# Kernel tuning notes

Measured on AMD Instinct MI355X. Metric: run time of the kernel, lower is better.

Reference implementation:

```python
import jax, jax.numpy as jnp
import numpy as np

N_NODES = 100000
N_EDGES = 1600000
N_GRAPHS = 256
HIDDEN = 256
ADD_FEATURES = 7
BN_EPS = 1e-5


def setup_inputs() -> dict:
    key = jax.random.key(0)
    ks = jax.random.split(key, 12)
    x = jax.random.normal(ks[0], (N_NODES, 1), dtype=jnp.float32)
    edge_index = jax.random.randint(ks[1], (2, N_EDGES), 0, N_NODES, dtype=jnp.int32)
    batch = jnp.sort(jax.random.randint(ks[2], (N_NODES,), 0, N_GRAPHS, dtype=jnp.int32))
    y_feat = jax.random.normal(ks[3], (N_GRAPHS, ADD_FEATURES), dtype=jnp.float32)
    # learned parameters
    W_conv = jax.random.normal(ks[4], (1, HIDDEN), dtype=jnp.float32) * 0.5
    b_conv = jnp.zeros((HIDDEN,), dtype=jnp.float32)
    gamma = jnp.ones((HIDDEN,), dtype=jnp.float32)
    beta = jnp.zeros((HIDDEN,), dtype=jnp.float32)
    W1 = jax.random.normal(ks[5], (HIDDEN + ADD_FEATURES, 128), dtype=jnp.float32) * (1.0 / np.sqrt(HIDDEN + ADD_FEATURES))
    b1 = jnp.zeros((128,), dtype=jnp.float32)
    W2 = jax.random.normal(ks[6], (128, 2), dtype=jnp.float32) * (1.0 / np.sqrt(128))
    b2 = jnp.zeros((2,), dtype=jnp.float32)
    return {"x": x, "edge_index": edge_index, "batch": batch, "y_feat": y_feat,
            "W_conv": W_conv, "b_conv": b_conv, "gamma": gamma, "beta": beta,
            "W1": W1, "b1": b1, "W2": W2, "b2": b2}


def _gcn_conv(x, W, b, edge_index, n_nodes):
    # PyG GCNConv: add self-loops, symmetric normalization D^-1/2 (A+I) D^-1/2 (x W) + b
    loop = jnp.arange(n_nodes, dtype=edge_index.dtype)
    src = jnp.concatenate([edge_index[0], loop])
    dst = jnp.concatenate([edge_index[1], loop])
    deg = jax.ops.segment_sum(jnp.ones_like(dst, dtype=x.dtype), dst, num_segments=n_nodes)
    dinv = jnp.where(deg > 0, jax.lax.rsqrt(jnp.maximum(deg, 1e-12)), 0.0)
    norm = dinv[src] * dinv[dst]                      # [E+N]
    xw = x @ W                                        # [N, H]
    msg = xw[src] * norm[:, None]                     # gather [E+N, H]
    return jax.ops.segment_sum(msg, dst, num_segments=n_nodes) + b


def reference(x, edge_index, batch, y_feat, W_conv, b_conv, gamma, beta, W1, b1, W2, b2):
    n_nodes = x.shape[0]
    h = _gcn_conv(x, W_conv, b_conv, edge_index, n_nodes)      # [N, 256]
    h = jax.nn.gelu(h, approximate=False)
    # BatchNorm over nodes (training-mode batch stats, biased variance, eps=1e-5)
    mean = jnp.mean(h, axis=0)
    var = jnp.mean(jnp.square(h - mean), axis=0)
    h = (h - mean) * jax.lax.rsqrt(var + BN_EPS) * gamma + beta
    # global mean pool by graph id
    sums = jax.ops.segment_sum(h, batch, num_segments=N_GRAPHS)           # [G, 256]
    counts = jax.ops.segment_sum(jnp.ones((n_nodes,), h.dtype), batch, num_segments=N_GRAPHS)
    pooled = sums / jnp.maximum(counts, 1.0)[:, None]
    g = jnp.concatenate([pooled, y_feat], axis=1)               # [G, 263]
    g = jax.nn.gelu(g @ W1 + b1, approximate=False)             # [G, 128]
    out = jax.nn.sigmoid(g @ W2 + b2)                           # [G, 2]
    return out
```

## Files before the change

### kernel.cpp

```cpp
#include <hip/hip_runtime.h>
#include <hip/hip_bf16.h>

#define HID 256
#define ADDF 7
#define MLP1 128
#define BN_EPS 1e-5f
#define NREP 8

#define NB 512
#define BW 196
#define BCAP 4096
#define NW 4
#define NR 8
#define NCHUNK 512

__device__ __forceinline__ float gelu_fast(float z) {
    float z2 = z * z;
    float y2 = z * fmaf(0.07135481627f, z2, 1.59576912161f);
    float u  = __expf(fminf(y2, 80.0f));
    return z * u * __builtin_amdgcn_rcpf(u + 1.0f);
}

__global__ __launch_bounds__(256) void k_hist(
        const int* __restrict__ dst, int* __restrict__ hist,
        float* __restrict__ zbase, int zcount, int E, int nchunk, int cpx, int PC) {
    __shared__ int h[NW][NB];
    const int t = threadIdx.x;
    const int bid = blockIdx.x;

    for (int gt = bid * 256 + t; gt < zcount; gt += (int)gridDim.x * 256) zbase[gt] = 0.0f;

    const int m = (bid & 7) * cpx + (bid >> 3);
    for (int k = t; k < NW * NB; k += 256) (&h[0][0])[k] = 0;
    __syncthreads();

    if (m < nchunk) {
        const int s0 = m * PC;
        const int e0 = min(s0 + PC, E);
        const int w = t >> 6;
        const bool al = ((((uintptr_t)(dst + s0)) & 15) == 0);
        const int n4 = al ? ((e0 - s0) >> 2) : 0;
        const int4* dst4 = (const int4*)(dst + s0);
        for (int q = t; q < n4; q += 256) {
            int4 d = dst4[q];
            atomicAdd(&h[w][d.x / BW], 1);
            atomicAdd(&h[w][d.y / BW], 1);
            atomicAdd(&h[w][d.z / BW], 1);
            atomicAdd(&h[w][d.w / BW], 1);
        }
        for (int i = s0 + (n4 << 2) + t; i < e0; i += 256)
            atomicAdd(&h[w][dst[i] / BW], 1);
        __syncthreads();
        for (int b = t; b < NB; b += 256)
            hist[(size_t)m * NB + b] = h[0][b] + h[1][b] + h[2][b] + h[3][b];
    }
}

__global__ __launch_bounds__(64) void k_scan(
        int* __restrict__ hist, int* __restrict__ binCur,
        const int* __restrict__ batch, int* __restrict__ cnt,
        int nchunk, int N, int G) {
    const int bin = blockIdx.x;
    const int lane = threadIdx.x;
    __shared__ int bounds[2];

    if (bin < G && lane < 2) {
        int target = bin + lane;
        int lo = 0, hi = N;
        while (lo < hi) { int mid = (lo + hi) >> 1; if (batch[mid] < target) lo = mid + 1; else hi = mid; }
        bounds[lane] = lo;
    }

    const int per = (nchunk + 63) / 64;
    const int m0 = lane * per;
    const int m1 = min(m0 + per, nchunk);
    int sum = 0;
    for (int m = m0; m < m1; ++m) sum += hist[(size_t)m * NB + bin];

    int incl = sum;
    #pragma unroll
    for (int d = 1; d < 64; d <<= 1) {
        int o = __shfl_up(incl, d);
        if (lane >= d) incl += o;
    }
    const int total = __shfl(incl, 63);
    int run = bin * BCAP + (incl - sum);
    for (int m = m0; m < m1; ++m) {
        int c = hist[(size_t)m * NB + bin];
        hist[(size_t)m * NB + bin] = run;
        run += c;
    }
    if (lane == 63) binCur[bin] = bin * BCAP + total;

    __syncthreads();
    if (bin < G && lane == 0) cnt[bin] = bounds[1] - bounds[0];
}

__global__ __launch_bounds__(256) void k_store(
        const int* __restrict__ src, const int* __restrict__ dst,
        const int* __restrict__ hist, int* __restrict__ recs,
        int E, int nchunk, int cpx, int PC) {
    __shared__ int cur[NB];
    const int t = threadIdx.x;
    const int m = ((int)blockIdx.x & 7) * cpx + ((int)blockIdx.x >> 3);
    if (m >= nchunk) return;

    {
        const int4* hrow = (const int4*)(hist + (size_t)m * NB);
        int4* cur4 = (int4*)cur;
        for (int b = t; b < NB / 4; b += 256) cur4[b] = hrow[b];
    }
    __syncthreads();

    const int s0 = m * PC;
    const int e0 = min(s0 + PC, E);
    const bool al = (((((uintptr_t)(dst + s0)) | ((uintptr_t)(src + s0))) & 15) == 0);
    const int n4 = al ? ((e0 - s0) >> 2) : 0;
    const int4* dst4 = (const int4*)(dst + s0);
    const int4* src4 = (const int4*)(src + s0);
    for (int q = t; q < n4; q += 256) {
        int4 d = dst4[q];
        int4 s = src4[q];
        int bin, pos;
        bin = d.x / BW; pos = atomicAdd(&cur[bin], 1); recs[pos] = ((d.x - bin * BW) << 17) | s.x;
        bin = d.y / BW; pos = atomicAdd(&cur[bin], 1); recs[pos] = ((d.y - bin * BW) << 17) | s.y;
        bin = d.z / BW; pos = atomicAdd(&cur[bin], 1); recs[pos] = ((d.z - bin * BW) << 17) | s.z;
        bin = d.w / BW; pos = atomicAdd(&cur[bin], 1); recs[pos] = ((d.w - bin * BW) << 17) | s.w;
    }
    for (int i = s0 + (n4 << 2) + t; i < e0; i += 256) {
        int d = dst[i];
        int bin = d / BW;
        int pos = atomicAdd(&cur[bin], 1);
        recs[pos] = ((d - bin * BW) << 17) | src[i];
    }
}

__global__ __launch_bounds__(1024) void k_degv(
        const int* __restrict__ recs, const int* __restrict__ binCur,
        const float* __restrict__ x, float* __restrict__ dinv, float* __restrict__ v, int N) {
    __shared__ int degL[NR][BW];
    const int b = blockIdx.x;
    const int t = threadIdx.x;
    const int rp = t >> 7;
    for (int k = t; k < NR * BW; k += 1024) (&degL[0][0])[k] = 0;
    __syncthreads();

    const int start = b * BCAP;
    const int end   = binCur[b];
    const int n4 = (end - start) >> 2;
    const int4* r4 = (const int4*)(recs + start);
    for (int q = t; q < n4; q += 1024) {
        int4 r = r4[q];
        atomicAdd(&degL[rp][r.x >> 17], 1);
        atomicAdd(&degL[rp][r.y >> 17], 1);
        atomicAdd(&degL[rp][r.z >> 17], 1);
        atomicAdd(&degL[rp][r.w >> 17], 1);
    }
    for (int i = start + (n4 << 2) + t; i < end; i += 1024)
        atomicAdd(&degL[rp][recs[i] >> 17], 1);
    __syncthreads();

    int node = b * BW + t;
    if (t < BW && node < N) {
        int d = 0;
        #pragma unroll
        for (int r = 0; r < NR; ++r) d += degL[r][t];
        float di = rsqrtf((float)d + 1.0f);
        dinv[node] = di;
        v[node]    = di * x[node];
    }
}

__global__ __launch_bounds__(1024) void k_agg_gelu(
        const int* __restrict__ recs, const int* __restrict__ binCur,
        const float* __restrict__ v, const float* __restrict__ dinv,
        const int* __restrict__ batch,
        const float* __restrict__ Wc, const float* __restrict__ bc,
        float* __restrict__ Sgj, float* __restrict__ Trep, float* __restrict__ T2rep, int N) {
    __shared__ float aggL[NR][BW];
    __shared__ float sh_s[BW];
    __shared__ int   sh_b[BW];
    const int b = blockIdx.x;
    const int t = threadIdx.x;
    const int rp = t >> 7;
    for (int k = t; k < NR * BW; k += 1024) (&aggL[0][0])[k] = 0.0f;
    __syncthreads();

    const int start = b * BCAP;
    const int end   = binCur[b];
    const int n4 = (end - start) >> 2;
    const int4* r4 = (const int4*)(recs + start);
    for (int q = t; q < n4; q += 1024) {
        int4 r = r4[q];
        atomicAdd(&aggL[rp][r.x >> 17], v[r.x & 0x1FFFF]);
        atomicAdd(&aggL[rp][r.y >> 17], v[r.y & 0x1FFFF]);
        atomicAdd(&aggL[rp][r.z >> 17], v[r.z & 0x1FFFF]);
        atomicAdd(&aggL[rp][r.w >> 17], v[r.w & 0x1FFFF]);
    }
    for (int i = start + (n4 << 2) + t; i < end; i += 1024) {
        int rec = recs[i];
        atomicAdd(&aggL[rp][rec >> 17], v[rec & 0x1FFFF]);
    }
    __syncthreads();

    const int node0 = b * BW;
    const int count = min(BW, N - node0);
    if (count <= 0) return;

    if (t < count) {
        int node = node0 + t;
        float a = 0.f;
        #pragma unroll
        for (int r = 0; r < NR; ++r) a += aggL[r][t];
        sh_s[t] = dinv[node] * (a + v[node]);
        sh_b[t] = batch[node];
    }
    __syncthreads();

    const int f = t & 255;
    const int qg = t >> 8;
    const int nbeg = qg * 49;
    const int nend = min(nbeg + 49, count);
    if (nbeg < nend) {
        const float wa = Wc[f];
        const float wb = bc[f];
        float tsum = 0.f, t2sum = 0.f, gsum = 0.f;
        int gid = sh_b[nbeg];
        int n = nbeg;
        for (; n + 2 <= nend; n += 2) {
            float h0 = gelu_fast(fmaf(sh_s[n],     wa, wb));
            float h1 = gelu_fast(fmaf(sh_s[n + 1], wa, wb));
            int b0 = sh_b[n], b1v = sh_b[n + 1];
            tsum += h0 + h1; t2sum += fmaf(h0, h0, h1 * h1);
            if (b0 != gid)  { atomicAdd(&Sgj[gid * HID + f], gsum); gsum = 0.f; gid = b0; }
            gsum += h0;
            if (b1v != gid) { atomicAdd(&Sgj[gid * HID + f], gsum); gsum = 0.f; gid = b1v; }
            gsum += h1;
        }
        if (n < nend) {
            float h0 = gelu_fast(fmaf(sh_s[n], wa, wb));
            tsum += h0; t2sum += h0 * h0;
            int b0 = sh_b[n];
            if (b0 != gid) { atomicAdd(&Sgj[gid * HID + f], gsum); gsum = 0.f; gid = b0; }
            gsum += h0;
        }
        atomicAdd(&Sgj[gid * HID + f], gsum);
        const int r = (b * 4 + qg) & (NREP - 1);
        atomicAdd(&Trep [r * HID + f], tsum);
        atomicAdd(&T2rep[r * HID + f], t2sum);
    }
}

__global__ __launch_bounds__(HID) void k_pool_mlp(
        const float* __restrict__ Sgj, const float* __restrict__ Trep, const float* __restrict__ T2rep,
        const int* __restrict__ cnt, const float* __restrict__ gamma, const float* __restrict__ beta,
        const float* __restrict__ yfeat,
        const float* __restrict__ W1, const float* __restrict__ b1,
        const float* __restrict__ W2, const float* __restrict__ b2,
        float* __restrict__ out, int N) {
    __shared__ float gv[HID + ADDF];
    __shared__ float hid[MLP1];
    const int g = blockIdx.x;
    const int t = threadIdx.x;

    float Ts = 0.f, T2s = 0.f;
    #pragma unroll
    for (int r = 0; r < NREP; ++r) { Ts += Trep[r * HID + t]; T2s += T2rep[r * HID + t]; }
    float invN = 1.0f / (float)N;
    float mean = Ts * invN;
    float var  = fmaf(-mean, mean, T2s * invN);
    float rinv = rsqrtf(var + BN_EPS);
    float c = (float)max(cnt[g], 1);
    gv[t] = (Sgj[g * HID + t] / c - mean) * rinv * gamma[t] + beta[t];
    if (t < ADDF) gv[HID + t] = yfeat[g * ADDF + t];
    __syncthreads();

    if (t < MLP1) {
        float acc = b1[t];
        #pragma unroll 8
        for (int k = 0; k < HID + ADDF; ++k)
            acc = fmaf(gv[k], W1[k * MLP1 + t], acc);
        hid[t] = gelu_fast(acc);
    }
    __syncthreads();

    if (t < 2) {
        float o = b2[t];
        for (int k = 0; k < MLP1; ++k)
            o = fmaf(hid[k], W2[k * 2 + t], o);
        out[g * 2 + t] = 1.0f / (1.0f + expf(-o));
    }
}

__global__ void k_init_fb(float* zp, int nz, const int* __restrict__ batch,
                          int* __restrict__ cnt, int N, int G) {
    const int nzBlocks = (nz + 255) / 256;
    if ((int)blockIdx.x < nzBlocks) {
        int i = blockIdx.x * 256 + threadIdx.x;
        if (i < nz) zp[i] = 0.0f;
    } else {
        const int t = threadIdx.x;
        if (t < G) {
            int lo = 0, hi = N;
            while (lo < hi) { int mid = (lo + hi) >> 1; if (batch[mid] < t) lo = mid + 1; else hi = mid; }
            int start = lo;
            lo = 0; hi = N;
            while (lo < hi) { int mid = (lo + hi) >> 1; if (batch[mid] < t + 1) lo = mid + 1; else hi = mid; }
            cnt[t] = lo - start;
        }
    }
}
__global__ void k_zero(float* p, int n) {
    for (int i = blockIdx.x * blockDim.x + threadIdx.x; i < n; i += gridDim.x * blockDim.x)
        p[i] = 0.0f;
}
__global__ void k_deg_fb(const int* __restrict__ dst, float* __restrict__ deg, int E) {
    int i = blockIdx.x * blockDim.x + threadIdx.x;
    if (i < E) atomicAdd(&deg[dst[i]], 1.0f);
}
__global__ void k_dinv_fb(float* __restrict__ deg, const float* __restrict__ x,
                          float* __restrict__ v, int N) {
    int i = blockIdx.x * blockDim.x + threadIdx.x;
    if (i < N) { float di = rsqrtf(deg[i] + 1.0f); deg[i] = di; v[i] = di * x[i]; }
}
__global__ void k_scatter_fb(const int* __restrict__ src, const int* __restrict__ dst,
                             const float* __restrict__ v, float* __restrict__ agg, int E) {
    int i = blockIdx.x * blockDim.x + threadIdx.x;
    if (i < E) atomicAdd(&agg[dst[i]], v[src[i]]);
}
#define CHUNK_FB 64
__global__ __launch_bounds__(HID) void k_gelu_fb(
        const float* __restrict__ v, const float* __restrict__ dinv,
        const float* __restrict__ agg, const int* __restrict__ batch,
        const float* __restrict__ Wc, const float* __restrict__ bc,
        float* __restrict__ Sgj, float* __restrict__ Trep, float* __restrict__ T2rep, int N) {
    __shared__ float sh_s[CHUNK_FB];
    __shared__ int   sh_b[CHUNK_FB];
    const int j = threadIdx.x;
    const int base = blockIdx.x * CHUNK_FB;
    const int count = min(CHUNK_FB, N - base);
    if (j < count) {
        int i = base + j;
        sh_s[j] = dinv[i] * (agg[i] + v[i]);
        sh_b[j] = batch[i];
    }
    __syncthreads();
    const float a = Wc[j];
    const float b = bc[j];
    float tsum = 0.f, t2sum = 0.f, gsum = 0.f;
    int gid = sh_b[0];
    for (int n = 0; n < count; ++n) {
        float h = gelu_fast(fmaf(sh_s[n], a, b));
        tsum += h; t2sum += h * h;
        int bg = sh_b[n];
        if (bg != gid) { atomicAdd(&Sgj[gid * HID + j], gsum); gsum = 0.f; gid = bg; }
        gsum += h;
    }
    atomicAdd(&Sgj[gid * HID + j], gsum);
    const int r = blockIdx.x & (NREP - 1);
    atomicAdd(&Trep [r * HID + j], tsum);
    atomicAdd(&T2rep[r * HID + j], t2sum);
}

extern "C" void kernel_launch(void* const* d_in, const int* in_sizes, int n_in,
                              void* d_out, int out_size, void* d_ws, size_t ws_size,
                              hipStream_t stream) {
    const float* x     = (const float*)d_in[0];
    const int*   edge  = (const int*)  d_in[1];
    const int*   batch = (const int*)  d_in[2];
    const float* yfeat = (const float*)d_in[3];
    const float* Wc    = (const float*)d_in[4];
    const float* bc    = (const float*)d_in[5];
    const float* gamma = (const float*)d_in[6];
    const float* beta  = (const float*)d_in[7];
    const float* W1    = (const float*)d_in[8];
    const float* b1    = (const float*)d_in[9];
    const float* W2    = (const float*)d_in[10];
    const float* b2    = (const float*)d_in[11];
    float* out = (float*)d_out;

    const int N = in_sizes[0];
    const int E = in_sizes[1] / 2;
    const int G = in_sizes[3] / ADDF;

    const int* srcIdx = edge;
    const int* dstIdx = edge + E;

    const int PC     = (((E + NCHUNK - 1) / NCHUNK) + 3) & ~3;
    const int nchunk = (E + PC - 1) / PC;
    const int cpx    = (NCHUNK + 7) / 8;

    float* ws     = (float*)d_ws;
    float* Sgj    = ws;
    float* Trep   = Sgj + (size_t)G * HID;
    float* T2rep  = Trep + NREP * HID;
    int*   cnt    = (int*)(T2rep + NREP * HID);
    int*   binCur = cnt + G;
    float* dinv   = (float*)(binCur + NB);
    float* v      = dinv + (size_t)NB * BW;
    int*   hist   = (int*)(v + (size_t)NB * BW);
    int*   recs   = hist + (size_t)NCHUNK * NB;

    const size_t headF  = (size_t)G * HID + 2 * NREP * HID + G + NB + 2 * (size_t)NB * BW;
    const size_t needT1 = (headF + (size_t)NCHUNK * NB + (size_t)NB * BCAP) * 4;
    const int zeroCount = G * HID + 2 * NREP * HID;

    if (ws_size >= needT1 && N <= NB * BW && G <= NB) {
        k_hist<<<NCHUNK, 256, 0, stream>>>(dstIdx, hist, Sgj, zeroCount, E, nchunk, cpx, PC);
        k_scan<<<NB, 64, 0, stream>>>(hist, binCur, batch, cnt, nchunk, N, G);
        k_store<<<NCHUNK, 256, 0, stream>>>(srcIdx, dstIdx, hist, recs, E, nchunk, cpx, PC);
        k_degv<<<NB, 1024, 0, stream>>>(recs, binCur, x, dinv, v, N);
        k_agg_gelu<<<NB, 1024, 0, stream>>>(recs, binCur, v, dinv, batch, Wc, bc, Sgj, Trep, T2rep, N);
        k_pool_mlp<<<G, HID, 0, stream>>>(Sgj, Trep, T2rep, cnt, gamma, beta, yfeat, W1, b1, W2, b2, out, N);
    } else {
        float* degA = (float*)(binCur + NB);
        float* vA   = degA + N;
        float* aggA = vA + N;
        const int initBlocks = (zeroCount + 255) / 256 + 1;
        k_init_fb<<<initBlocks, 256, 0, stream>>>(Sgj, zeroCount, batch, cnt, N, G);
        k_zero<<<512, 256, 0, stream>>>(degA, N);
        k_zero<<<512, 256, 0, stream>>>(aggA, N);
        k_deg_fb<<<(E + 255) / 256, 256, 0, stream>>>(dstIdx, degA, E);
        k_dinv_fb<<<(N + 255) / 256, 256, 0, stream>>>(degA, x, vA, N);
        k_scatter_fb<<<(E + 255) / 256, 256, 0, stream>>>(srcIdx, dstIdx, vA, aggA, E);
        k_gelu_fb<<<(N + CHUNK_FB - 1) / CHUNK_FB, HID, 0, stream>>>(vA, degA, aggA, batch, Wc, bc, Sgj, Trep, T2rep, N);
        k_pool_mlp<<<G, HID, 0, stream>>>(Sgj, Trep, T2rep, cnt, gamma, beta, yfeat, W1, b1, W2, b2, out, N);
    }
}
```

Baseline: 72.59 us.

## Accumulate graph pooling sums in shared memory and replicate global accumulators

In the aggregation+GELU kernel, per-graph sums for the first four graphs a block touches are now accumulated in shared memory, as are the BatchNorm sum and sum-of-squares. Each block then writes its pooled partials to one of 8 global replicas with plain stores, and adds its statistics to one of 64 replicas with atomics. The pool/MLP kernel reduces across these replicas. The goal is fewer contended global float atomics. In exchange, a much larger workspace must be zeroed each call. The plain stores also assume no two blocks with the same replica index cover the same graph, which holds only when graphs are small relative to the block stride.

```diff
diff --git a/kernel.cpp b/kernel.cpp
--- a/kernel.cpp
+++ b/kernel.cpp
@@ -5,7 +5,8 @@
 #define ADDF 7
 #define MLP1 128
 #define BN_EPS 1e-5f
-#define NREP 8
+#define NSREP 8
+#define NTREP 64
 
 #define NB 512
 #define BW 196
@@ -176,14 +177,20 @@
         const float* __restrict__ v, const float* __restrict__ dinv,
         const int* __restrict__ batch,
         const float* __restrict__ Wc, const float* __restrict__ bc,
-        float* __restrict__ Sgj, float* __restrict__ Trep, float* __restrict__ T2rep, int N) {
+        float* __restrict__ Sgj8, float* __restrict__ Trep, float* __restrict__ T2rep,
+        int N, int G) {
     __shared__ float aggL[NR][BW];
     __shared__ float sh_s[BW];
     __shared__ int   sh_b[BW];
+    __shared__ float shG[4][HID];
+    __shared__ float shT[HID], shT2[HID];
     const int b = blockIdx.x;
     const int t = threadIdx.x;
     const int rp = t >> 7;
     for (int k = t; k < NR * BW; k += 1024) (&aggL[0][0])[k] = 0.0f;
+    for (int k = t; k < 4 * HID; k += 1024) (&shG[0][0])[k] = 0.0f;
+    if (t < HID) shT[t] = 0.0f;
+    else if (t < 2 * HID) shT2[t - HID] = 0.0f;
     __syncthreads();
 
     const int start = b * BCAP;
@@ -217,6 +224,7 @@
     }
     __syncthreads();
 
+    const int g0 = sh_b[0];
     const int f = t & 255;
     const int qg = t >> 8;
     const int nbeg = qg * 49;
@@ -232,46 +240,80 @@
             float h1 = gelu_fast(fmaf(sh_s[n + 1], wa, wb));
             int b0 = sh_b[n], b1v = sh_b[n + 1];
             tsum += h0 + h1; t2sum += fmaf(h0, h0, h1 * h1);
-            if (b0 != gid)  { atomicAdd(&Sgj[gid * HID + f], gsum); gsum = 0.f; gid = b0; }
+            if (b0 != gid) {
+                int sl = gid - g0;
+                if (sl < 4) atomicAdd(&shG[sl][f], gsum);
+                else atomicAdd(&Sgj8[((size_t)(b & 7) * G + gid) * HID + f], gsum);
+                gsum = 0.f; gid = b0;
+            }
             gsum += h0;
-            if (b1v != gid) { atomicAdd(&Sgj[gid * HID + f], gsum); gsum = 0.f; gid = b1v; }
+            if (b1v != gid) {
+                int sl = gid - g0;
+                if (sl < 4) atomicAdd(&shG[sl][f], gsum);
+                else atomicAdd(&Sgj8[((size_t)(b & 7) * G + gid) * HID + f], gsum);
+                gsum = 0.f; gid = b1v;
+            }
             gsum += h1;
         }
         if (n < nend) {
             float h0 = gelu_fast(fmaf(sh_s[n], wa, wb));
             tsum += h0; t2sum += h0 * h0;
             int b0 = sh_b[n];
-            if (b0 != gid) { atomicAdd(&Sgj[gid * HID + f], gsum); gsum = 0.f; gid = b0; }
+            if (b0 != gid) {
+                int sl = gid - g0;
+                if (sl < 4) atomicAdd(&shG[sl][f], gsum);
+                else atomicAdd(&Sgj8[((size_t)(b & 7) * G + gid) * HID + f], gsum);
+                gsum = 0.f; gid = b0;
+            }
             gsum += h0;
         }
-        atomicAdd(&Sgj[gid * HID + f], gsum);
-        const int r = (b * 4 + qg) & (NREP - 1);
-        atomicAdd(&Trep [r * HID + f], tsum);
-        atomicAdd(&T2rep[r * HID + f], t2sum);
+        {
+            int sl = gid - g0;
+            if (sl < 4) atomicAdd(&shG[sl][f], gsum);
+            else atomicAdd(&Sgj8[((size_t)(b & 7) * G + gid) * HID + f], gsum);
+        }
+        atomicAdd(&shT[f],  tsum);
+        atomicAdd(&shT2[f], t2sum);
+    }
+    __syncthreads();
+
+    {
+        const int sl = t >> 8;
+        const int ff = t & 255;
+        const int gmax = sh_b[count - 1];
+        const int g = g0 + sl;
+        if (g <= gmax && g < G)
+            Sgj8[((size_t)(b & 7) * G + g) * HID + ff] = shG[sl][ff];
+        if (t < HID)            atomicAdd(&Trep [(b & (NTREP - 1)) * HID + t], shT[t]);
+        else if (t < 2 * HID)   atomicAdd(&T2rep[(b & (NTREP - 1)) * HID + (t - HID)], shT2[t - HID]);
     }
 }
 
 __global__ __launch_bounds__(HID) void k_pool_mlp(
-        const float* __restrict__ Sgj, const float* __restrict__ Trep, const float* __restrict__ T2rep,
+        const float* __restrict__ Sgj8, const float* __restrict__ Trep, const float* __restrict__ T2rep,
         const int* __restrict__ cnt, const float* __restrict__ gamma, const float* __restrict__ beta,
         const float* __restrict__ yfeat,
         const float* __restrict__ W1, const float* __restrict__ b1,
         const float* __restrict__ W2, const float* __restrict__ b2,
-        float* __restrict__ out, int N) {
+        float* __restrict__ out, int N, int G) {
     __shared__ float gv[HID + ADDF];
     __shared__ float hid[MLP1];
     const int g = blockIdx.x;
     const int t = threadIdx.x;
 
     float Ts = 0.f, T2s = 0.f;
+    #pragma unroll 8
+    for (int r = 0; r < NTREP; ++r) { Ts += Trep[r * HID + t]; T2s += T2rep[r * HID + t]; }
+    float Sg = 0.f;
     #pragma unroll
-    for (int r = 0; r < NREP; ++r) { Ts += Trep[r * HID + t]; T2s += T2rep[r * HID + t]; }
+    for (int r = 0; r < NSREP; ++r) Sg += Sgj8[((size_t)r * G + g) * HID + t];
+
     float invN = 1.0f / (float)N;
     float mean = Ts * invN;
     float var  = fmaf(-mean, mean, T2s * invN);
     float rinv = rsqrtf(var + BN_EPS);
     float c = (float)max(cnt[g], 1);
-    gv[t] = (Sgj[g * HID + t] / c - mean) * rinv * gamma[t] + beta[t];
+    gv[t] = (Sg / c - mean) * rinv * gamma[t] + beta[t];
     if (t < ADDF) gv[HID + t] = yfeat[g * ADDF + t];
     __syncthreads();
 
@@ -333,7 +375,8 @@
         const float* __restrict__ v, const float* __restrict__ dinv,
         const float* __restrict__ agg, const int* __restrict__ batch,
         const float* __restrict__ Wc, const float* __restrict__ bc,
-        float* __restrict__ Sgj, float* __restrict__ Trep, float* __restrict__ T2rep, int N) {
+        float* __restrict__ Sgj8, float* __restrict__ Trep, float* __restrict__ T2rep,
+        int N, int G) {
     __shared__ float sh_s[CHUNK_FB];
     __shared__ int   sh_b[CHUNK_FB];
     const int j = threadIdx.x;
@@ -349,15 +392,16 @@
     const float b = bc[j];
     float tsum = 0.f, t2sum = 0.f, gsum = 0.f;
     int gid = sh_b[0];
+    const size_t rb = (size_t)(blockIdx.x & 7) * G;
     for (int n = 0; n < count; ++n) {
         float h = gelu_fast(fmaf(sh_s[n], a, b));
         tsum += h; t2sum += h * h;
         int bg = sh_b[n];
-        if (bg != gid) { atomicAdd(&Sgj[gid * HID + j], gsum); gsum = 0.f; gid = bg; }
+        if (bg != gid) { atomicAdd(&Sgj8[(rb + gid) * HID + j], gsum); gsum = 0.f; gid = bg; }
         gsum += h;
     }
-    atomicAdd(&Sgj[gid * HID + j], gsum);
-    const int r = blockIdx.x & (NREP - 1);
+    atomicAdd(&Sgj8[(rb + gid) * HID + j], gsum);
+    const int r = blockIdx.x & (NTREP - 1);
     atomicAdd(&Trep [r * HID + j], tsum);
     atomicAdd(&T2rep[r * HID + j], t2sum);
 }
@@ -391,39 +435,39 @@
     const int cpx    = (NCHUNK + 7) / 8;
 
     float* ws     = (float*)d_ws;
-    float* Sgj    = ws;
-    float* Trep   = Sgj + (size_t)G * HID;
-    float* T2rep  = Trep + NREP * HID;
-    int*   cnt    = (int*)(T2rep + NREP * HID);
+    float* Sgj8   = ws;
+    float* Trep   = Sgj8 + (size_t)NSREP * G * HID;
+    float* T2rep  = Trep + NTREP * HID;
+    int*   cnt    = (int*)(T2rep + NTREP * HID);
     int*   binCur = cnt + G;
     float* dinv   = (float*)(binCur + NB);
     float* v      = dinv + (size_t)NB * BW;
     int*   hist   = (int*)(v + (size_t)NB * BW);
     int*   recs   = hist + (size_t)NCHUNK * NB;
 
-    const size_t headF  = (size_t)G * HID + 2 * NREP * HID + G + NB + 2 * (size_t)NB * BW;
+    const size_t headF  = (size_t)NSREP * G * HID + 2 * NTREP * HID + G + NB + 2 * (size_t)NB * BW;
     const size_t needT1 = (headF + (size_t)NCHUNK * NB + (size_t)NB * BCAP) * 4;
-    const int zeroCount = G * HID + 2 * NREP * HID;
+    const int zeroCount = NSREP * G * HID + 2 * NTREP * HID;
 
     if (ws_size >= needT1 && N <= NB * BW && G <= NB) {
-        k_hist<<<NCHUNK, 256, 0, stream>>>(dstIdx, hist, Sgj, zeroCount, E, nchunk, cpx, PC);
+        k_hist<<<NCHUNK, 256, 0, stream>>>(dstIdx, hist, Sgj8, zeroCount, E, nchunk, cpx, PC);
         k_scan<<<NB, 64, 0, stream>>>(hist, binCur, batch, cnt, nchunk, N, G);
         k_store<<<NCHUNK, 256, 0, stream>>>(srcIdx, dstIdx, hist, recs, E, nchunk, cpx, PC);
         k_degv<<<NB, 1024, 0, stream>>>(recs, binCur, x, dinv, v, N);
-        k_agg_gelu<<<NB, 1024, 0, stream>>>(recs, binCur, v, dinv, batch, Wc, bc, Sgj, Trep, T2rep, N);
-        k_pool_mlp<<<G, HID, 0, stream>>>(Sgj, Trep, T2rep, cnt, gamma, beta, yfeat, W1, b1, W2, b2, out, N);
+        k_agg_gelu<<<NB, 1024, 0, stream>>>(recs, binCur, v, dinv, batch, Wc, bc, Sgj8, Trep, T2rep, N, G);
+        k_pool_mlp<<<G, HID, 0, stream>>>(Sgj8, Trep, T2rep, cnt, gamma, beta, yfeat, W1, b1, W2, b2, out, N, G);
     } else {
         float* degA = (float*)(binCur + NB);
         float* vA   = degA + N;
         float* aggA = vA + N;
         const int initBlocks = (zeroCount + 255) / 256 + 1;
-        k_init_fb<<<initBlocks, 256, 0, stream>>>(Sgj, zeroCount, batch, cnt, N, G);
+        k_init_fb<<<initBlocks, 256, 0, stream>>>(Sgj8, zeroCount, batch, cnt, N, G);
         k_zero<<<512, 256, 0, stream>>>(degA, N);
         k_zero<<<512, 256, 0, stream>>>(aggA, N);
         k_deg_fb<<<(E + 255) / 256, 256, 0, stream>>>(dstIdx, degA, E);
         k_dinv_fb<<<(N + 255) / 256, 256, 0, stream>>>(degA, x, vA, N);
         k_scatter_fb<<<(E + 255) / 256, 256, 0, stream>>>(srcIdx, dstIdx, vA, aggA, E);
-        k_gelu_fb<<<(N + CHUNK_FB - 1) / CHUNK_FB, HID, 0, stream>>>(vA, degA, aggA, batch, Wc, bc, Sgj, Trep, T2rep, N);
-        k_pool_mlp<<<G, HID, 0, stream>>>(Sgj, Trep, T2rep, cnt, gamma, beta, yfeat, W1, b1, W2, b2, out, N);
-    }
-}
+        k_gelu_fb<<<(N + CHUNK_FB - 1) / CHUNK_FB, HID, 0, stream>>>(vA, degA, aggA, batch, Wc, bc, Sgj8, Trep, T2rep, N, G);
+        k_pool_mlp<<<G, HID, 0, stream>>>(Sgj8, Trep, T2rep, cnt, gamma, beta, yfeat, W1, b1, W2, b2, out, N, G);
+    }
+}
```

After: 81.99 us. 1.13x slower.

## Replace global histogram/scan/store bucketing with per-chunk local sort placement

Applied to the files above, without the earlier changes.

Merges the histogram, global scan and scatter kernels into one k_place kernel. It loads each edge chunk into LDS, does a block-local histogram and scan, and writes the records sorted by bin within the chunk's own region, along with a packed offset/length table. The degree and aggregation kernels then read each bin's records by walking all 512 chunk segments through that table, so the cross-block scan pass and two launches disappear. In exchange, the per-bin reads become short, scattered per-thread serial loops instead of contiguous int4 streams. It also adds XCD-aware block remapping.

```diff
diff --git a/kernel.cpp b/kernel.cpp
--- a/kernel.cpp
+++ b/kernel.cpp
@@ -9,10 +9,8 @@
 
 #define NB 512
 #define BW 196
-#define BCAP 4096
-#define NW 4
-#define NR 8
 #define NCHUNK 512
+#define PCMAX 3200
 
 __device__ __forceinline__ float gelu_fast(float z) {
     float z2 = z * z;
@@ -21,185 +19,152 @@
     return z * u * __builtin_amdgcn_rcpf(u + 1.0f);
 }
 
-__global__ __launch_bounds__(256) void k_hist(
-        const int* __restrict__ dst, int* __restrict__ hist,
-        float* __restrict__ zbase, int zcount, int E, int nchunk, int cpx, int PC) {
-    __shared__ int h[NW][NB];
+__device__ __forceinline__ int xcd_map(int bid) {
+    return (bid & 7) * 64 + (bid >> 3);
+}
+
+__global__ __launch_bounds__(512) void k_place(
+        const int* __restrict__ src, const int* __restrict__ dst,
+        int* __restrict__ packed, int* __restrict__ recs,
+        float* __restrict__ zbase, int zcount, int E, int PC) {
+    __shared__ int eD[PCMAX];
+    __shared__ int eS[PCMAX];
+    __shared__ int h[8][NB];
+    __shared__ int wsum[8];
     const int t = threadIdx.x;
-    const int bid = blockIdx.x;
-
-    for (int gt = bid * 256 + t; gt < zcount; gt += (int)gridDim.x * 256) zbase[gt] = 0.0f;
-
-    const int m = (bid & 7) * cpx + (bid >> 3);
-    for (int k = t; k < NW * NB; k += 256) (&h[0][0])[k] = 0;
-    __syncthreads();
-
-    if (m < nchunk) {
-        const int s0 = m * PC;
-        const int e0 = min(s0 + PC, E);
-        const int w = t >> 6;
-        const bool al = ((((uintptr_t)(dst + s0)) & 15) == 0);
-        const int n4 = al ? ((e0 - s0) >> 2) : 0;
-        const int4* dst4 = (const int4*)(dst + s0);
-        for (int q = t; q < n4; q += 256) {
-            int4 d = dst4[q];
-            atomicAdd(&h[w][d.x / BW], 1);
-            atomicAdd(&h[w][d.y / BW], 1);
-            atomicAdd(&h[w][d.z / BW], 1);
-            atomicAdd(&h[w][d.w / BW], 1);
-        }
-        for (int i = s0 + (n4 << 2) + t; i < e0; i += 256)
-            atomicAdd(&h[w][dst[i] / BW], 1);
-        __syncthreads();
-        for (int b = t; b < NB; b += 256)
-            hist[(size_t)m * NB + b] = h[0][b] + h[1][b] + h[2][b] + h[3][b];
-    }
-}
-
-__global__ __launch_bounds__(64) void k_scan(
-        int* __restrict__ hist, int* __restrict__ binCur,
-        const int* __restrict__ batch, int* __restrict__ cnt,
-        int nchunk, int N, int G) {
-    const int bin = blockIdx.x;
-    const int lane = threadIdx.x;
-    __shared__ int bounds[2];
-
-    if (bin < G && lane < 2) {
-        int target = bin + lane;
-        int lo = 0, hi = N;
-        while (lo < hi) { int mid = (lo + hi) >> 1; if (batch[mid] < target) lo = mid + 1; else hi = mid; }
-        bounds[lane] = lo;
-    }
-
-    const int per = (nchunk + 63) / 64;
-    const int m0 = lane * per;
-    const int m1 = min(m0 + per, nchunk);
-    int sum = 0;
-    for (int m = m0; m < m1; ++m) sum += hist[(size_t)m * NB + bin];
-
-    int incl = sum;
+    const int lane = t & 63;
+    const int w = t >> 6;
+
+    {
+        int gt = (int)blockIdx.x * 512 + t;
+        if (gt < zcount) zbase[gt] = 0.0f;
+    }
+
+    const int m = xcd_map((int)blockIdx.x);
+    const int s0 = m * PC;
+    const int e0 = min(s0 + PC, E);
+    const int len0 = max(e0 - s0, 0);
+
+    for (int k = t; k < 8 * NB; k += 512) (&h[0][0])[k] = 0;
+
+    if (len0 > 0) {
+        const bool al = (((((uintptr_t)(dst + s0)) | ((uintptr_t)(src + s0))) & 15) == 0);
+        const int n4 = al ? (len0 >> 2) : 0;
+        const int4* d4 = (const int4*)(dst + s0);
+        const int4* s4 = (const int4*)(src + s0);
+        for (int q = t; q < n4; q += 512) {
+            ((int4*)eD)[q] = d4[q];
+            ((int4*)eS)[q] = s4[q];
+        }
+        for (int i = (n4 << 2) + t; i < len0; i += 512) {
+            eD[i] = dst[s0 + i];
+            eS[i] = src[s0 + i];
+        }
+    }
+    __syncthreads();
+
+    for (int i = t; i < len0; i += 512)
+        atomicAdd(&h[w][eD[i] / BW], 1);
+    __syncthreads();
+
+    int tot = 0;
+    #pragma unroll
+    for (int ww = 0; ww < 8; ++ww) tot += h[ww][t];
+    int incl = tot;
     #pragma unroll
     for (int d = 1; d < 64; d <<= 1) {
         int o = __shfl_up(incl, d);
         if (lane >= d) incl += o;
     }
-    const int total = __shfl(incl, 63);
-    int run = bin * BCAP + (incl - sum);
-    for (int m = m0; m < m1; ++m) {
-        int c = hist[(size_t)m * NB + bin];
-        hist[(size_t)m * NB + bin] = run;
-        run += c;
-    }
-    if (lane == 63) binCur[bin] = bin * BCAP + total;
-
-    __syncthreads();
-    if (bin < G && lane == 0) cnt[bin] = bounds[1] - bounds[0];
-}
-
-__global__ __launch_bounds__(256) void k_store(
-        const int* __restrict__ src, const int* __restrict__ dst,
-        const int* __restrict__ hist, int* __restrict__ recs,
-        int E, int nchunk, int cpx, int PC) {
-    __shared__ int cur[NB];
+    if (lane == 63) wsum[w] = incl;
+    __syncthreads();
+    int pre = 0;
+    for (int ww = 0; ww < w; ++ww) pre += wsum[ww];
+    const int loc = pre + incl - tot;
+    packed[(size_t)m * NB + t] = loc | (tot << 16);
+
+    {
+        int run = s0 + loc;
+        #pragma unroll
+        for (int ww = 0; ww < 8; ++ww) { int c = h[ww][t]; h[ww][t] = run; run += c; }
+    }
+    __syncthreads();
+
+    for (int i = t; i < len0; i += 512) {
+        int d = eD[i];
+        int bin = d / BW;
+        int pos = atomicAdd(&h[w][bin], 1);
+        recs[pos] = ((d - bin * BW) << 17) | eS[i];
+    }
+}
+
+__global__ __launch_bounds__(512) void k_degv(
+        const int* __restrict__ packed, const int* __restrict__ recs,
+        const float* __restrict__ x, const int* __restrict__ batch,
+        float* __restrict__ dinv, float* __restrict__ v, int* __restrict__ cnt,
+        int N, int G, int PC) {
+    __shared__ int degL[4][BW];
+    __shared__ int bounds[2];
+    const int b = xcd_map((int)blockIdx.x);
     const int t = threadIdx.x;
-    const int m = ((int)blockIdx.x & 7) * cpx + ((int)blockIdx.x >> 3);
-    if (m >= nchunk) return;
+    for (int k = t; k < 4 * BW; k += 512) (&degL[0][0])[k] = 0;
+
+    if (t < 2 && b < G) {
+        int target = b + t;
+        int lo = 0, hi = N;
+        while (lo < hi) { int mid = (lo + hi) >> 1; if (batch[mid] < target) lo = mid + 1; else hi = mid; }
+        bounds[t] = lo;
+    }
+    __syncthreads();
 
     {
-        const int4* hrow = (const int4*)(hist + (size_t)m * NB);
-        int4* cur4 = (int4*)cur;
-        for (int b = t; b < NB / 4; b += 256) cur4[b] = hrow[b];
-    }
-    __syncthreads();
-
-    const int s0 = m * PC;
-    const int e0 = min(s0 + PC, E);
-    const bool al = (((((uintptr_t)(dst + s0)) | ((uintptr_t)(src + s0))) & 15) == 0);
-    const int n4 = al ? ((e0 - s0) >> 2) : 0;
-    const int4* dst4 = (const int4*)(dst + s0);
-    const int4* src4 = (const int4*)(src + s0);
-    for (int q = t; q < n4; q += 256) {
-        int4 d = dst4[q];
-        int4 s = src4[q];
-        int bin, pos;
-        bin = d.x / BW; pos = atomicAdd(&cur[bin], 1); recs[pos] = ((d.x - bin * BW) << 17) | s.x;
-        bin = d.y / BW; pos = atomicAdd(&cur[bin], 1); recs[pos] = ((d.y - bin * BW) << 17) | s.y;
-        bin = d.z / BW; pos = atomicAdd(&cur[bin], 1); recs[pos] = ((d.z - bin * BW) << 17) | s.z;
-        bin = d.w / BW; pos = atomicAdd(&cur[bin], 1); recs[pos] = ((d.w - bin * BW) << 17) | s.w;
-    }
-    for (int i = s0 + (n4 << 2) + t; i < e0; i += 256) {
-        int d = dst[i];
-        int bin = d / BW;
-        int pos = atomicAdd(&cur[bin], 1);
-        recs[pos] = ((d - bin * BW) << 17) | src[i];
-    }
-}
-
-__global__ __launch_bounds__(1024) void k_degv(
-        const int* __restrict__ recs, const int* __restrict__ binCur,
-        const float* __restrict__ x, float* __restrict__ dinv, float* __restrict__ v, int N) {
-    __shared__ int degL[NR][BW];
-    const int b = blockIdx.x;
-    const int t = threadIdx.x;
-    const int rp = t >> 7;
-    for (int k = t; k < NR * BW; k += 1024) (&degL[0][0])[k] = 0;
-    __syncthreads();
-
-    const int start = b * BCAP;
-    const int end   = binCur[b];
-    const int n4 = (end - start) >> 2;
-    const int4* r4 = (const int4*)(recs + start);
-    for (int q = t; q < n4; q += 1024) {
-        int4 r = r4[q];
-        atomicAdd(&degL[rp][r.x >> 17], 1);
-        atomicAdd(&degL[rp][r.y >> 17], 1);
-        atomicAdd(&degL[rp][r.z >> 17], 1);
-        atomicAdd(&degL[rp][r.w >> 17], 1);
-    }
-    for (int i = start + (n4 << 2) + t; i < end; i += 1024)
-        atomicAdd(&degL[rp][recs[i] >> 17], 1);
-    __syncthreads();
-
-    int node = b * BW + t;
-    if (t < BW && node < N) {
-        int d = 0;
-        #pragma unroll
-        for (int r = 0; r < NR; ++r) d += degL[r][t];
-        float di = rsqrtf((float)d + 1.0f);
-        dinv[node] = di;
-        v[node]    = di * x[node];
-    }
+        int p = packed[(size_t)t * NB + b];
+        int base = t * PC + (p & 0xFFFF);
+        int len = ((unsigned)p) >> 16;
+        const int rp = t >> 7;
+        for (int k = 0; k < len; ++k)
+            atomicAdd(&degL[rp][recs[base + k] >> 17], 1);
+    }
+    __syncthreads();
+
+    if (t < BW) {
+        int node = b * BW + t;
+        if (node < N) {
+            int d = degL[0][t] + degL[1][t] + degL[2][t] + degL[3][t];
+            float di = rsqrtf((float)d + 1.0f);
+            dinv[node] = di;
+            v[node]    = di * x[node];
+        }
+    }
+    if (t == 0 && b < G) cnt[b] = bounds[1] - bounds[0];
 }
 
 __global__ __launch_bounds__(1024) void k_agg_gelu(
-        const int* __restrict__ recs, const int* __restrict__ binCur,
+        const int* __restrict__ packed, const int* __restrict__ recs,
         const float* __restrict__ v, const float* __restrict__ dinv,
         const int* __restrict__ batch,
         const float* __restrict__ Wc, const float* __restrict__ bc,
-        float* __restrict__ Sgj, float* __restrict__ Trep, float* __restrict__ T2rep, int N) {
-    __shared__ float aggL[NR][BW];
+        float* __restrict__ Sgj, float* __restrict__ Trep, float* __restrict__ T2rep,
+        int N, int G, int PC) {
+    __shared__ float aggL[8][BW];
     __shared__ float sh_s[BW];
     __shared__ int   sh_b[BW];
-    const int b = blockIdx.x;
+    const int b = xcd_map((int)blockIdx.x);
     const int t = threadIdx.x;
-    const int rp = t >> 7;
-    for (int k = t; k < NR * BW; k += 1024) (&aggL[0][0])[k] = 0.0f;
-    __syncthreads();
-
-    const int start = b * BCAP;
-    const int end   = binCur[b];
-    const int n4 = (end - start) >> 2;
-    const int4* r4 = (const int4*)(recs + start);
-    for (int q = t; q < n4; q += 1024) {
-        int4 r = r4[q];
-        atomicAdd(&aggL[rp][r.x >> 17], v[r.x & 0x1FFFF]);
-        atomicAdd(&aggL[rp][r.y >> 17], v[r.y & 0x1FFFF]);
-        atomicAdd(&aggL[rp][r.z >> 17], v[r.z & 0x1FFFF]);
-        atomicAdd(&aggL[rp][r.w >> 17], v[r.w & 0x1FFFF]);
-    }
-    for (int i = start + (n4 << 2) + t; i < end; i += 1024) {
-        int rec = recs[i];
-        atomicAdd(&aggL[rp][rec >> 17], v[rec & 0x1FFFF]);
+    for (int k = t; k < 8 * BW; k += 1024) (&aggL[0][0])[k] = 0.0f;
+    __syncthreads();
+
+    {
+        const int m = t & 511;
+        const int half = t >> 9;
+        int p = packed[(size_t)m * NB + b];
+        int base = m * PC + (p & 0xFFFF);
+        int len = ((unsigned)p) >> 16;
+        const int rp = t >> 7;
+        for (int k = half; k < len; k += 2) {
+            int rec = recs[base + k];
+            atomicAdd(&aggL[rp][rec >> 17], v[rec & 0x1FFFF]);
+        }
     }
     __syncthreads();
 
@@ -211,7 +176,7 @@
         int node = node0 + t;
         float a = 0.f;
         #pragma unroll
-        for (int r = 0; r < NR; ++r) a += aggL[r][t];
+        for (int r = 0; r < 8; ++r) a += aggL[r][t];
         sh_s[t] = dinv[node] * (a + v[node]);
         sh_b[t] = batch[node];
     }
@@ -245,7 +210,7 @@
             gsum += h0;
         }
         atomicAdd(&Sgj[gid * HID + f], gsum);
-        const int r = (b * 4 + qg) & (NREP - 1);
+        const int r = ((int)blockIdx.x * 4 + qg) & (NREP - 1);
         atomicAdd(&Trep [r * HID + f], tsum);
         atomicAdd(&T2rep[r * HID + f], t2sum);
     }
@@ -386,36 +351,36 @@
     const int* srcIdx = edge;
     const int* dstIdx = edge + E;
 
-    const int PC     = (((E + NCHUNK - 1) / NCHUNK) + 3) & ~3;
-    const int nchunk = (E + PC - 1) / PC;
-    const int cpx    = (NCHUNK + 7) / 8;
+    const int PC = (((E + NCHUNK - 1) / NCHUNK) + 3) & ~3;
 
     float* ws     = (float*)d_ws;
     float* Sgj    = ws;
     float* Trep   = Sgj + (size_t)G * HID;
     float* T2rep  = Trep + NREP * HID;
     int*   cnt    = (int*)(T2rep + NREP * HID);
-    int*   binCur = cnt + G;
-    float* dinv   = (float*)(binCur + NB);
+    float* dinv   = (float*)(cnt + G);
     float* v      = dinv + (size_t)NB * BW;
-    int*   hist   = (int*)(v + (size_t)NB * BW);
-    int*   recs   = hist + (size_t)NCHUNK * NB;
-
-    const size_t headF  = (size_t)G * HID + 2 * NREP * HID + G + NB + 2 * (size_t)NB * BW;
-    const size_t needT1 = (headF + (size_t)NCHUNK * NB + (size_t)NB * BCAP) * 4;
+    int*   packed = (int*)(v + (size_t)NB * BW);
+    int*   recs   = packed + (size_t)NCHUNK * NB;
+
+    const size_t headF  = (size_t)G * HID + 2 * NREP * HID + G + 2 * (size_t)NB * BW;
+    const size_t needT1 = (headF + (size_t)NCHUNK * NB + (size_t)NCHUNK * PC) * 4;
     const int zeroCount = G * HID + 2 * NREP * HID;
 
-    if (ws_size >= needT1 && N <= NB * BW && G <= NB) {
-        k_hist<<<NCHUNK, 256, 0, stream>>>(dstIdx, hist, Sgj, zeroCount, E, nchunk, cpx, PC);
-        k_scan<<<NB, 64, 0, stream>>>(hist, binCur, batch, cnt, nchunk, N, G);
-        k_store<<<NCHUNK, 256, 0, stream>>>(srcIdx, dstIdx, hist, recs, E, nchunk, cpx, PC);
-        k_degv<<<NB, 1024, 0, stream>>>(recs, binCur, x, dinv, v, N);
-        k_agg_gelu<<<NB, 1024, 0, stream>>>(recs, binCur, v, dinv, batch, Wc, bc, Sgj, Trep, T2rep, N);
+    if (ws_size >= needT1 && N <= NB * BW && G <= 256 && PC <= PCMAX && N < (1 << 17)) {
+        k_place<<<NCHUNK, 512, 0, stream>>>(srcIdx, dstIdx, packed, recs, Sgj, zeroCount, E, PC);
+        k_degv<<<NB, 512, 0, stream>>>(packed, recs, x, batch, dinv, v, cnt, N, G, PC);
+        k_agg_gelu<<<NB, 1024, 0, stream>>>(packed, recs, v, dinv, batch, Wc, bc, Sgj, Trep, T2rep, N, G, PC);
         k_pool_mlp<<<G, HID, 0, stream>>>(Sgj, Trep, T2rep, cnt, gamma, beta, yfeat, W1, b1, W2, b2, out, N);
     } else {
-        float* degA = (float*)(binCur + NB);
-        float* vA   = degA + N;
-        float* aggA = vA + N;
+        float* degA = dinv;
+        float* vA   = v;
+        float* aggA = (float*)packed;
+        if ((size_t)N > (size_t)NB * BW) {
+            degA = (float*)(cnt + G);
+            vA   = degA + N;
+            aggA = vA + N;
+        }
         const int initBlocks = (zeroCount + 255) / 256 + 1;
         k_init_fb<<<initBlocks, 256, 0, stream>>>(Sgj, zeroCount, batch, cnt, N, G);
         k_zero<<<512, 256, 0, stream>>>(degA, N);
```

Result: slower. 74.36 us (+2.4%).
